# Performance work log

Measured on AMD Instinct MI355X. Metric: run time of the kernel, lower is better.

## Reference

```python
import jax, jax.numpy as jnp
import numpy as np


def _xavier(key, shape):
    fan_out, fan_in = shape
    lim = float(np.sqrt(6.0 / (fan_in + fan_out)))
    return jax.random.uniform(key, shape, jnp.float32, -lim, lim)


def setup_inputs() -> dict:
    B, I, H, P = 8192, 1024, 1024, 2048
    key = jax.random.key(0)
    ks = jax.random.split(key, 12)
    return {
        "x": jax.random.normal(ks[0], (B, I), jnp.float32),
        "hidden": jax.random.normal(ks[1], (B, H), jnp.float32),
        "persistent_memory": jax.random.normal(ks[2], (B, P), jnp.float32),
        # attention_gate: Linear(H,H), 'gate' bias init = -0.1
        "Wa": _xavier(ks[3], (H, H)), "ba": jnp.full((H,), -0.1, jnp.float32),
        # reset/update/new gates: Linear(I+H, H), 'gate' bias init = -0.1
        "Wr": _xavier(ks[4], (H, I + H)), "br": jnp.full((H,), -0.1, jnp.float32),
        "Wu": _xavier(ks[5], (H, I + H)), "bu": jnp.full((H,), -0.1, jnp.float32),
        "Wn": _xavier(ks[6], (H, I + H)), "bn": jnp.full((H,), -0.1, jnp.float32),
        # memory read/write/address: Linear(H,P), zero bias; forget bias = 1.0
        "Wread": _xavier(ks[7], (P, H)), "bread": jnp.zeros((P,), jnp.float32),
        "Wwrite": _xavier(ks[8], (P, H)), "bwrite": jnp.zeros((P,), jnp.float32),
        "Wforget": _xavier(ks[9], (P, H)), "bforget": jnp.ones((P,), jnp.float32),
        "Waddr": _xavier(ks[10], (P, H)), "baddr": jnp.zeros((P,), jnp.float32),
        "connection_strength": jnp.ones((H,), jnp.float32),
        "connection_decay": jnp.full((1,), 0.99, jnp.float32),
        "connection_history": jnp.zeros((H,), jnp.float32),  # buffer, starts at 0
    }


def reference(x, hidden, persistent_memory, Wa, ba, Wr, br, Wu, bu, Wn, bn,
              Wread, bread, Wwrite, bwrite, Wforget, bforget, Waddr, baddr,
              connection_strength, connection_decay, connection_history):
    H = hidden.shape[1]
    # update_connections (reward=None): history*decay + detached mean(|h|) over batch
    activity = jax.lax.stop_gradient(jnp.mean(jnp.abs(hidden), axis=0))  # [H]
    ch = connection_history * connection_decay + activity
    cs = connection_strength * jax.nn.sigmoid(ch)  # [H]

    attention = jax.nn.sigmoid(hidden @ Wa.T + ba)
    ha = hidden * attention
    combined = jnp.concatenate([x, ha], axis=1)
    reset = combined @ Wr.T + br
    update = combined @ Wu.T + bu
    combined_reset = jnp.concatenate([x, reset * ha], axis=1)
    new = combined_reset @ Wn.T + bn
    # neuromodulators=None: apply_neuromodulation returns gates UNACTIVATED (faithful)
    hidden_new = (1.0 - update) * hidden + update * new * cs[None, :]  # [B,H]

    addr = jax.nn.softmax(hidden_new @ Waddr.T + baddr, axis=1)        # [B,P]
    read = jax.nn.sigmoid(hidden_new @ Wread.T + bread)
    write = jax.nn.sigmoid(hidden_new @ Wwrite.T + bwrite)
    forget = jax.nn.sigmoid(hidden_new @ Wforget.T + bforget)

    # F.linear with ones(P,H)/H weight == row-mean of hidden_new broadcast to P
    hp = jnp.mean(hidden_new, axis=1, keepdims=True)                   # [B,1]
    memory_new = forget * persistent_memory + write * hp * addr        # [B,P]
    memory_read_content = read * memory_new
    # F.linear with ones(H,P)/P weight == row-mean over P broadcast to H
    hidden_final = hidden_new + jnp.mean(memory_read_content, axis=1, keepdims=True)
    return hidden_final, memory_new
```

## Files before the change

kernel.cpp:

```cpp
#include <hip/hip_runtime.h>

typedef unsigned short u16;
typedef short bfrag __attribute__((ext_vector_type(8)));
typedef float f32x4 __attribute__((ext_vector_type(4)));
typedef const __attribute__((address_space(1))) unsigned int* gp1_t;
typedef __attribute__((address_space(3))) unsigned int* lp3_t;

#define B_ 8192
#define H_ 1024
#define P_ 2048

__device__ __forceinline__ u16 f2bf(float f) {
  unsigned u = __builtin_bit_cast(unsigned, f);
  u += 0x7fffu + ((u >> 16) & 1u);
  return (u16)(u >> 16);
}
__device__ __forceinline__ float bf2f(u16 s) {
  return __builtin_bit_cast(float, (unsigned)s << 16);
}
__device__ __forceinline__ float sigm(float v) { return 1.f / (1.f + __expf(-v)); }


__global__ void k_hidact(const float* __restrict__ hidden, u16* __restrict__ hB,
                         float* __restrict__ act) {
  const int t = threadIdx.x;
  const int r0 = blockIdx.x * 16;
  float s00 = 0, s01 = 0, s10 = 0, s11 = 0;
  for (int r = 0; r < 16; ++r) {
    const float* q = hidden + (size_t)(r0 + r) * H_;
    u16* o = hB + (size_t)(r0 + r) * H_;
    float2 v0 = *(const float2*)&q[2 * t];
    float2 v1 = *(const float2*)&q[512 + 2 * t];
    s00 += fabsf(v0.x); s01 += fabsf(v0.y);
    s10 += fabsf(v1.x); s11 += fabsf(v1.y);
    ushort2 o0, o1;
    o0.x = f2bf(v0.x); o0.y = f2bf(v0.y);
    o1.x = f2bf(v1.x); o1.y = f2bf(v1.y);
    *(ushort2*)&o[2 * t] = o0;
    *(ushort2*)&o[512 + 2 * t] = o1;
  }
  atomicAdd(&act[2 * t], s00); atomicAdd(&act[2 * t + 1], s01);
  atomicAdd(&act[512 + 2 * t], s10); atomicAdd(&act[512 + 2 * t + 1], s11);
}

__global__ void k_cs(const float* __restrict__ act, const float* __restrict__ strength,
                     const float* __restrict__ decay, const float* __restrict__ hist,
                     float* __restrict__ cs) {
  int h = blockIdx.x * 256 + threadIdx.x;
  float ch = hist[h] * decay[0] + act[h] * (1.f / (float)B_);
  cs[h] = strength[h] * sigm(ch);
}

struct ConvPs {
  const float* s[9];
  u16* d[9];
  int n4[9];
};

__global__ void k_conv9(ConvPs p) {
  const int e = blockIdx.y;
  const int n4 = p.n4[e];
  const float4* s = (const float4*)p.s[e];
  ushort4* d = (ushort4*)p.d[e];
  for (int i = blockIdx.x * 256 + threadIdx.x; i < n4; i += 2048 * 256) {
    float4 v = s[i];
    ushort4 o;
    o.x = f2bf(v.x); o.y = f2bf(v.y); o.z = f2bf(v.z); o.w = f2bf(v.w);
    d[i] = o;
  }
}

__global__ void k_rowmean(const float* __restrict__ hn, float* __restrict__ hp) {
  int row = blockIdx.x * 4 + (threadIdx.x >> 6);
  int lane = threadIdx.x & 63;
  const float4* p4 = (const float4*)(hn + (size_t)row * H_);
  float s = 0.f;
#pragma unroll
  for (int c = 0; c < 4; ++c) {
    float4 v = p4[lane + c * 64];
    s += v.x + v.y + v.z + v.w;
  }
#pragma unroll
  for (int o = 32; o; o >>= 1) s += __shfl_down(s, o);
  if (lane == 0) hp[row] = s * (1.f / (float)H_);
}


struct GemmPs {
  const u16* Bm[4];
  const float* bias[4];
  const float* hidden;
  const float* update;
  const float* cs;
  const u16* haB;
  u16* rhaB;
  float* out_f1;
  float* hn_f32;
  u16* hn_bf16;
  u16* haB_out;
  u16* out_b[4];
};

template <int EPI>
__device__ __forceinline__ void epiV(int row, int col0, f32x4 v, int z, const GemmPs& e) {
  if constexpr (EPI == 1) {
    float4 bi = *(const float4*)&e.bias[0][col0];
    size_t i = (size_t)row * H_ + col0;
    float4 hd = *(const float4*)&e.hidden[i];
    ushort4 o;
    o.x = f2bf(hd.x * sigm(v[0] + bi.x));
    o.y = f2bf(hd.y * sigm(v[1] + bi.y));
    o.z = f2bf(hd.z * sigm(v[2] + bi.z));
    o.w = f2bf(hd.w * sigm(v[3] + bi.w));
    *(ushort4*)&e.haB_out[i] = o;
  } else if constexpr (EPI == 2) {
    size_t i = (size_t)row * H_ + col0;
    if (z == 0) {
      float4 bi = *(const float4*)&e.bias[0][col0];
      ushort4 h = *(const ushort4*)&e.haB[i];
      ushort4 o;
      o.x = f2bf((v[0] + bi.x) * bf2f(h.x));
      o.y = f2bf((v[1] + bi.y) * bf2f(h.y));
      o.z = f2bf((v[2] + bi.z) * bf2f(h.z));
      o.w = f2bf((v[3] + bi.w) * bf2f(h.w));
      *(ushort4*)&e.rhaB[i] = o;
    } else {
      float4 bi = *(const float4*)&e.bias[1][col0];
      float4 o;
      o.x = v[0] + bi.x; o.y = v[1] + bi.y; o.z = v[2] + bi.z; o.w = v[3] + bi.w;
      *(float4*)&e.out_f1[i] = o;
    }
  } else if constexpr (EPI == 3) {
    float4 bi = *(const float4*)&e.bias[0][col0];
    size_t i = (size_t)row * H_ + col0;
    float4 u4 = *(const float4*)&e.update[i];
    float4 hd = *(const float4*)&e.hidden[i];
    float4 c4 = *(const float4*)&e.cs[col0];
    float4 hn;
    hn.x = (1.f - u4.x) * hd.x + u4.x * (v[0] + bi.x) * c4.x;
    hn.y = (1.f - u4.y) * hd.y + u4.y * (v[1] + bi.y) * c4.y;
    hn.z = (1.f - u4.z) * hd.z + u4.z * (v[2] + bi.z) * c4.z;
    hn.w = (1.f - u4.w) * hd.w + u4.w * (v[3] + bi.w) * c4.w;
    *(float4*)&e.hn_f32[i] = hn;
    ushort4 o;
    o.x = f2bf(hn.x); o.y = f2bf(hn.y); o.z = f2bf(hn.z); o.w = f2bf(hn.w);
    *(ushort4*)&e.hn_bf16[i] = o;
  } else {
    float4 bi = *(const float4*)&e.bias[z][col0];
    ushort4 o;
    o.x = f2bf(v[0] + bi.x); o.y = f2bf(v[1] + bi.y);
    o.z = f2bf(v[2] + bi.z); o.w = f2bf(v[3] + bi.w);
    *(ushort4*)&e.out_b[z][(size_t)row * P_ + col0] = o;
  }
}


template <int EPI, int KB, int NT0, int NT1>
__global__ __launch_bounds__(256, 2) void gemm_bt(const u16* __restrict__ A0,
                                                  const u16* __restrict__ A1,
                                                  GemmPs e) {
  const int z = blockIdx.z;
  const u16* __restrict__ Bm = e.Bm[z];
  __shared__ u16 As[128 * 64];
  __shared__ u16 Bs[128 * 64];
  const int lane = threadIdx.x & 63;
  const int w = threadIdx.x >> 6;
  const int wr = w >> 1, wc = w & 1;
  const int m0 = blockIdx.x * 128, n0 = blockIdx.y * 128;

  f32x4 acc[4][4] = {};

  const int rA = lane >> 3;
  const int srcSlot8 = ((lane & 7) ^ (rA & 7)) << 3;
  const int g = lane >> 4;
  const int r15 = lane & 15;
  const int rx = lane & 7;

  const u16* pA0 = A0 + (size_t)(m0 + w * 32 + rA) * H_ + srcSlot8;
  const u16* pA1 = A1 + (size_t)(m0 + w * 32 + rA) * H_ + srcSlot8;
  const u16* pB  = Bm + (size_t)(n0 + w * 32 + rA) * KB + srcSlot8;

  auto ktile = [&](const u16* pAk, const u16* pBk) {
#pragma unroll
    for (int j = 0; j < 4; ++j) {
      __builtin_amdgcn_global_load_lds((gp1_t)(pAk + (size_t)(j * 8) * H_),
                                       (lp3_t)&As[(w * 32 + j * 8) * 64], 16, 0, 0);
      __builtin_amdgcn_global_load_lds((gp1_t)(pBk + (size_t)(j * 8) * KB),
                                       (lp3_t)&Bs[(w * 32 + j * 8) * 64], 16, 0, 0);
    }
    asm volatile("s_waitcnt vmcnt(0)" ::: "memory");
    __syncthreads();
#pragma unroll
    for (int kk = 0; kk < 2; ++kk) {
      const int cswz = (((g + kk * 4) ^ rx) << 3);
      bfrag af[4], bq[4];
#pragma unroll
      for (int i = 0; i < 4; ++i) {
        af[i] = *(const bfrag*)&As[(wr * 64 + i * 16 + r15) * 64 + cswz];
        bq[i] = *(const bfrag*)&Bs[(wc * 64 + i * 16 + r15) * 64 + cswz];
      }
#pragma unroll
      for (int mi = 0; mi < 4; ++mi)
#pragma unroll
        for (int ni = 0; ni < 4; ++ni)
          acc[mi][ni] = __builtin_amdgcn_mfma_f32_16x16x32_bf16(bq[ni], af[mi], acc[mi][ni], 0, 0, 0);
    }
    __syncthreads();
  };

  for (int t = 0; t < NT0; ++t) ktile(pA0 + t * 64, pB + t * 64);
  if constexpr (NT1 > 0)
    for (int t = 0; t < NT1; ++t) ktile(pA1 + t * 64, pB + (NT0 + t) * 64);

#pragma unroll
  for (int mi = 0; mi < 4; ++mi)
#pragma unroll
    for (int ni = 0; ni < 4; ++ni)
      epiV<EPI>(m0 + wr * 64 + mi * 16 + r15,
                n0 + wc * 64 + ni * 16 + g * 4, acc[mi][ni], z, e);
}


__global__ __launch_bounds__(256) void k_final(
    const u16* __restrict__ aL, const u16* __restrict__ rL,
    const u16* __restrict__ wL, const u16* __restrict__ fL,
    const float* __restrict__ pm, const float* __restrict__ hn,
    const float* __restrict__ hp, float* __restrict__ outH, float* __restrict__ outM) {
  __shared__ float red[8];
  const int row = blockIdx.x, t = threadIdx.x;
  const size_t base = (size_t)row * P_ + t * 8;

  ushort4 a0 = *(const ushort4*)&aL[base];
  ushort4 a1 = *(const ushort4*)&aL[base + 4];
  float av[8] = {bf2f(a0.x), bf2f(a0.y), bf2f(a0.z), bf2f(a0.w),
                 bf2f(a1.x), bf2f(a1.y), bf2f(a1.z), bf2f(a1.w)};
  float lm = av[0];
#pragma unroll
  for (int j = 1; j < 8; ++j) lm = fmaxf(lm, av[j]);
#pragma unroll
  for (int o = 32; o; o >>= 1) lm = fmaxf(lm, __shfl_xor(lm, o));
  if ((t & 63) == 0) red[t >> 6] = lm;
  __syncthreads();
  const float bmax = fmaxf(fmaxf(red[0], red[1]), fmaxf(red[2], red[3]));

  float ev[8];
  float ls = 0.f;
#pragma unroll
  for (int j = 0; j < 8; ++j) { ev[j] = __expf(av[j] - bmax); ls += ev[j]; }
#pragma unroll
  for (int o = 32; o; o >>= 1) ls += __shfl_xor(ls, o);
  if ((t & 63) == 0) red[4 + (t >> 6)] = ls;
  __syncthreads();
  const float inv = 1.f / (red[4] + red[5] + red[6] + red[7]);
  const float hpv = hp[row];

  ushort4 r0 = *(const ushort4*)&rL[base], r1 = *(const ushort4*)&rL[base + 4];
  ushort4 w0 = *(const ushort4*)&wL[base], w1 = *(const ushort4*)&wL[base + 4];
  ushort4 f0 = *(const ushort4*)&fL[base], f1 = *(const ushort4*)&fL[base + 4];
  float4 p0 = *(const float4*)&pm[base], p1 = *(const float4*)&pm[base + 4];
  float rv[8] = {bf2f(r0.x), bf2f(r0.y), bf2f(r0.z), bf2f(r0.w),
                 bf2f(r1.x), bf2f(r1.y), bf2f(r1.z), bf2f(r1.w)};
  float wv[8] = {bf2f(w0.x), bf2f(w0.y), bf2f(w0.z), bf2f(w0.w),
                 bf2f(w1.x), bf2f(w1.y), bf2f(w1.z), bf2f(w1.w)};
  float fv[8] = {bf2f(f0.x), bf2f(f0.y), bf2f(f0.z), bf2f(f0.w),
                 bf2f(f1.x), bf2f(f1.y), bf2f(f1.z), bf2f(f1.w)};
  float pv[8] = {p0.x, p0.y, p0.z, p0.w, p1.x, p1.y, p1.z, p1.w};
  float mem[8];
  float rs = 0.f;
#pragma unroll
  for (int j = 0; j < 8; ++j) {
    mem[j] = sigm(fv[j]) * pv[j] + sigm(wv[j]) * hpv * (ev[j] * inv);
    rs += sigm(rv[j]) * mem[j];
  }
  float4 m0v = {mem[0], mem[1], mem[2], mem[3]};
  float4 m1v = {mem[4], mem[5], mem[6], mem[7]};
  *(float4*)&outM[base] = m0v;
  *(float4*)&outM[base + 4] = m1v;
#pragma unroll
  for (int o = 32; o; o >>= 1) rs += __shfl_xor(rs, o);
  __syncthreads();
  if ((t & 63) == 0) red[t >> 6] = rs;
  __syncthreads();
  const float mean = (red[0] + red[1] + red[2] + red[3]) * (1.f / (float)P_);
  const size_t hb = (size_t)row * H_ + t * 4;
  float4 h4 = *(const float4*)&hn[hb];
  h4.x += mean; h4.y += mean; h4.z += mean; h4.w += mean;
  *(float4*)&outH[hb] = h4;
}


extern "C" void kernel_launch(void* const* d_in, const int* in_sizes, int n_in,
                              void* d_out, int out_size, void* d_ws, size_t ws_size,
                              hipStream_t stream) {
  (void)in_sizes; (void)n_in; (void)out_size; (void)ws_size;
  const float* x       = (const float*)d_in[0];
  const float* hidden  = (const float*)d_in[1];
  const float* pm      = (const float*)d_in[2];
  const float* Wa      = (const float*)d_in[3];
  const float* ba      = (const float*)d_in[4];
  const float* Wr      = (const float*)d_in[5];
  const float* br      = (const float*)d_in[6];
  const float* Wu      = (const float*)d_in[7];
  const float* bu      = (const float*)d_in[8];
  const float* Wn      = (const float*)d_in[9];
  const float* bn      = (const float*)d_in[10];
  const float* Wread   = (const float*)d_in[11];
  const float* bread   = (const float*)d_in[12];
  const float* Wwrite  = (const float*)d_in[13];
  const float* bwrite  = (const float*)d_in[14];
  const float* Wforget = (const float*)d_in[15];
  const float* bforget = (const float*)d_in[16];
  const float* Waddr   = (const float*)d_in[17];
  const float* baddr   = (const float*)d_in[18];
  const float* cstr    = (const float*)d_in[19];
  const float* cdecay  = (const float*)d_in[20];
  const float* chist   = (const float*)d_in[21];

  char* wsp = (char*)d_ws;
  auto take = [&](size_t n) { char* p = wsp; wsp += (n + 255) & ~(size_t)255; return p; };
  float* act    = (float*)take((size_t)H_ * 4);
  float* cs     = (float*)take((size_t)H_ * 4);
  float* hp     = (float*)take((size_t)B_ * 4);
  u16* hiddenB  = (u16*)take((size_t)B_ * H_ * 2);
  u16* xB       = (u16*)take((size_t)B_ * H_ * 2);
  u16* haB      = (u16*)take((size_t)B_ * H_ * 2);
  u16* rhaB     = (u16*)take((size_t)B_ * H_ * 2);
  u16* WaB      = (u16*)take((size_t)H_ * H_ * 2);
  u16* WrB      = (u16*)take((size_t)H_ * 2048 * 2);
  u16* WuB      = (u16*)take((size_t)H_ * 2048 * 2);
  u16* WnB      = (u16*)take((size_t)H_ * 2048 * 2);
  u16* WadB     = (u16*)take((size_t)P_ * H_ * 2);
  u16* WrdB     = (u16*)take((size_t)P_ * H_ * 2);
  u16* WwrB     = (u16*)take((size_t)P_ * H_ * 2);
  u16* WfgB     = (u16*)take((size_t)P_ * H_ * 2);
  float* update = (float*)take((size_t)B_ * H_ * 4);
  float* hnf    = (float*)take((size_t)B_ * H_ * 4);
  u16* gAd      = (u16*)take((size_t)B_ * P_ * 2);
  u16* gRd      = (u16*)take((size_t)B_ * P_ * 2);
  u16* gWr      = (u16*)take((size_t)B_ * P_ * 2);
  u16* gFg      = (u16*)take((size_t)B_ * P_ * 2);

  float* outH = (float*)d_out;
  float* outM = outH + (size_t)B_ * H_;

  hipMemsetAsync(act, 0, (size_t)H_ * 4, stream);
  k_hidact<<<dim3(512), dim3(256), 0, stream>>>(hidden, hiddenB, act);
  k_cs<<<dim3(4), dim3(256), 0, stream>>>(act, cstr, cdecay, chist, cs);

  {
    ConvPs p;
    const float* ss[9] = {Wa, Wr, Wu, Wn, Waddr, Wread, Wwrite, Wforget, x};
    u16* dd[9] = {WaB, WrB, WuB, WnB, WadB, WrdB, WwrB, WfgB, xB};
    int nn[9] = {H_ * H_ / 4, H_ * 2048 / 4, H_ * 2048 / 4, H_ * 2048 / 4,
                 P_ * H_ / 4, P_ * H_ / 4, P_ * H_ / 4, P_ * H_ / 4, B_ * H_ / 4};
    for (int i = 0; i < 9; ++i) { p.s[i] = ss[i]; p.d[i] = dd[i]; p.n4[i] = nn[i]; }
    k_conv9<<<dim3(2048, 9), dim3(256), 0, stream>>>(p);
  }

  {
    GemmPs e{};
    e.Bm[0] = WaB; e.bias[0] = ba; e.hidden = hidden; e.haB_out = haB;
    gemm_bt<1, 1024, 16, 0><<<dim3(64, 8, 1), dim3(256), 0, stream>>>(hiddenB, hiddenB, e);
  }
  {
    GemmPs e{};
    e.Bm[0] = WrB; e.Bm[1] = WuB; e.bias[0] = br; e.bias[1] = bu;
    e.haB = haB; e.rhaB = rhaB; e.out_f1 = update;
    gemm_bt<2, 2048, 16, 16><<<dim3(64, 8, 2), dim3(256), 0, stream>>>(xB, haB, e);
  }
  {
    GemmPs e{};
    e.Bm[0] = WnB; e.bias[0] = bn; e.hidden = hidden; e.update = update; e.cs = cs;
    e.hn_f32 = hnf; e.hn_bf16 = hiddenB;
    gemm_bt<3, 2048, 16, 16><<<dim3(64, 8, 1), dim3(256), 0, stream>>>(xB, rhaB, e);
  }
  k_rowmean<<<dim3(2048), dim3(256), 0, stream>>>(hnf, hp);
  {
    GemmPs e{};
    e.Bm[0] = WadB; e.Bm[1] = WrdB; e.Bm[2] = WwrB; e.Bm[3] = WfgB;
    e.bias[0] = baddr; e.bias[1] = bread; e.bias[2] = bwrite; e.bias[3] = bforget;
    e.out_b[0] = gAd; e.out_b[1] = gRd; e.out_b[2] = gWr; e.out_b[3] = gFg;
    gemm_bt<4, 1024, 16, 0><<<dim3(64, 16, 4), dim3(256), 0, stream>>>(hiddenB, hiddenB, e);
  }
  k_final<<<dim3(B_), dim3(256), 0, stream>>>(gAd, gRd, gWr, gFg, pm, hnf, hp, outH, outM);
}
```

Before: 432.1 us.

## Fuse hidden_new row-mean into GEMM epilogue and drop fp32 hidden_new buffer

The hidden_new row-sum is now accumulated in the Wn GEMM epilogue through wave shuffles and atomics into hp, which removes the separate rowmean kernel. The fp32 hidden_new buffer is dropped, so the final kernel reads the bf16 copy instead. That saves a 32MB write and read but costs precision in hidden_final. The hidden activity/convert kernel is also reshaped to use float4 accesses with 64 rows per block.

Measured after the change: 403.5 us. 1.07x faster.

```diff
diff --git a/kernel.cpp b/kernel.cpp
--- a/kernel.cpp
+++ b/kernel.cpp
@@ -24,23 +24,18 @@
 __global__ void k_hidact(const float* __restrict__ hidden, u16* __restrict__ hB,
                          float* __restrict__ act) {
   const int t = threadIdx.x;
-  const int r0 = blockIdx.x * 16;
-  float s00 = 0, s01 = 0, s10 = 0, s11 = 0;
-  for (int r = 0; r < 16; ++r) {
-    const float* q = hidden + (size_t)(r0 + r) * H_;
-    u16* o = hB + (size_t)(r0 + r) * H_;
-    float2 v0 = *(const float2*)&q[2 * t];
-    float2 v1 = *(const float2*)&q[512 + 2 * t];
-    s00 += fabsf(v0.x); s01 += fabsf(v0.y);
-    s10 += fabsf(v1.x); s11 += fabsf(v1.y);
-    ushort2 o0, o1;
-    o0.x = f2bf(v0.x); o0.y = f2bf(v0.y);
-    o1.x = f2bf(v1.x); o1.y = f2bf(v1.y);
-    *(ushort2*)&o[2 * t] = o0;
-    *(ushort2*)&o[512 + 2 * t] = o1;
-  }
-  atomicAdd(&act[2 * t], s00); atomicAdd(&act[2 * t + 1], s01);
-  atomicAdd(&act[512 + 2 * t], s10); atomicAdd(&act[512 + 2 * t + 1], s11);
+  const int r0 = blockIdx.x * 64;
+  float s0 = 0, s1 = 0, s2 = 0, s3 = 0;
+  for (int r = 0; r < 64; ++r) {
+    const size_t i = (size_t)(r0 + r) * H_ + t * 4;
+    float4 v = *(const float4*)&hidden[i];
+    s0 += fabsf(v.x); s1 += fabsf(v.y); s2 += fabsf(v.z); s3 += fabsf(v.w);
+    ushort4 o;
+    o.x = f2bf(v.x); o.y = f2bf(v.y); o.z = f2bf(v.z); o.w = f2bf(v.w);
+    *(ushort4*)&hB[i] = o;
+  }
+  atomicAdd(&act[t * 4], s0); atomicAdd(&act[t * 4 + 1], s1);
+  atomicAdd(&act[t * 4 + 2], s2); atomicAdd(&act[t * 4 + 3], s3);
 }
 
 __global__ void k_cs(const float* __restrict__ act, const float* __restrict__ strength,
@@ -68,21 +63,6 @@
     o.x = f2bf(v.x); o.y = f2bf(v.y); o.z = f2bf(v.z); o.w = f2bf(v.w);
     d[i] = o;
   }
-}
-
-__global__ void k_rowmean(const float* __restrict__ hn, float* __restrict__ hp) {
-  int row = blockIdx.x * 4 + (threadIdx.x >> 6);
-  int lane = threadIdx.x & 63;
-  const float4* p4 = (const float4*)(hn + (size_t)row * H_);
-  float s = 0.f;
-#pragma unroll
-  for (int c = 0; c < 4; ++c) {
-    float4 v = p4[lane + c * 64];
-    s += v.x + v.y + v.z + v.w;
-  }
-#pragma unroll
-  for (int o = 32; o; o >>= 1) s += __shfl_down(s, o);
-  if (lane == 0) hp[row] = s * (1.f / (float)H_);
 }
 
 
@@ -95,14 +75,14 @@
   const u16* haB;
   u16* rhaB;
   float* out_f1;
-  float* hn_f32;
   u16* hn_bf16;
+  float* hp;
   u16* haB_out;
   u16* out_b[4];
 };
 
 template <int EPI>
-__device__ __forceinline__ void epiV(int row, int col0, f32x4 v, int z, const GemmPs& e) {
+__device__ __forceinline__ float epiV(int row, int col0, f32x4 v, int z, const GemmPs& e) {
   if constexpr (EPI == 1) {
     float4 bi = *(const float4*)&e.bias[0][col0];
     size_t i = (size_t)row * H_ + col0;
@@ -113,6 +93,7 @@
     o.z = f2bf(hd.z * sigm(v[2] + bi.z));
     o.w = f2bf(hd.w * sigm(v[3] + bi.w));
     *(ushort4*)&e.haB_out[i] = o;
+    return 0.f;
   } else if constexpr (EPI == 2) {
     size_t i = (size_t)row * H_ + col0;
     if (z == 0) {
@@ -130,27 +111,28 @@
       o.x = v[0] + bi.x; o.y = v[1] + bi.y; o.z = v[2] + bi.z; o.w = v[3] + bi.w;
       *(float4*)&e.out_f1[i] = o;
     }
+    return 0.f;
   } else if constexpr (EPI == 3) {
     float4 bi = *(const float4*)&e.bias[0][col0];
     size_t i = (size_t)row * H_ + col0;
     float4 u4 = *(const float4*)&e.update[i];
     float4 hd = *(const float4*)&e.hidden[i];
     float4 c4 = *(const float4*)&e.cs[col0];
-    float4 hn;
-    hn.x = (1.f - u4.x) * hd.x + u4.x * (v[0] + bi.x) * c4.x;
-    hn.y = (1.f - u4.y) * hd.y + u4.y * (v[1] + bi.y) * c4.y;
-    hn.z = (1.f - u4.z) * hd.z + u4.z * (v[2] + bi.z) * c4.z;
-    hn.w = (1.f - u4.w) * hd.w + u4.w * (v[3] + bi.w) * c4.w;
-    *(float4*)&e.hn_f32[i] = hn;
-    ushort4 o;
-    o.x = f2bf(hn.x); o.y = f2bf(hn.y); o.z = f2bf(hn.z); o.w = f2bf(hn.w);
+    float hx = (1.f - u4.x) * hd.x + u4.x * (v[0] + bi.x) * c4.x;
+    float hy = (1.f - u4.y) * hd.y + u4.y * (v[1] + bi.y) * c4.y;
+    float hz = (1.f - u4.z) * hd.z + u4.z * (v[2] + bi.z) * c4.z;
+    float hw = (1.f - u4.w) * hd.w + u4.w * (v[3] + bi.w) * c4.w;
+    ushort4 o;
+    o.x = f2bf(hx); o.y = f2bf(hy); o.z = f2bf(hz); o.w = f2bf(hw);
     *(ushort4*)&e.hn_bf16[i] = o;
+    return hx + hy + hz + hw;
   } else {
     float4 bi = *(const float4*)&e.bias[z][col0];
     ushort4 o;
     o.x = f2bf(v[0] + bi.x); o.y = f2bf(v[1] + bi.y);
     o.z = f2bf(v[2] + bi.z); o.w = f2bf(v[3] + bi.w);
     *(ushort4*)&e.out_b[z][(size_t)row * P_ + col0] = o;
+    return 0.f;
   }
 }
 
@@ -212,19 +194,38 @@
   if constexpr (NT1 > 0)
     for (int t = 0; t < NT1; ++t) ktile(pA1 + t * 64, pB + (NT0 + t) * 64);
 
-#pragma unroll
-  for (int mi = 0; mi < 4; ++mi)
-#pragma unroll
-    for (int ni = 0; ni < 4; ++ni)
-      epiV<EPI>(m0 + wr * 64 + mi * 16 + r15,
-                n0 + wc * 64 + ni * 16 + g * 4, acc[mi][ni], z, e);
+  if constexpr (EPI == 3) {
+    float rsum[4];
+#pragma unroll
+    for (int mi = 0; mi < 4; ++mi) {
+      rsum[mi] = 0.f;
+#pragma unroll
+      for (int ni = 0; ni < 4; ++ni)
+        rsum[mi] += epiV<EPI>(m0 + wr * 64 + mi * 16 + r15,
+                              n0 + wc * 64 + ni * 16 + g * 4, acc[mi][ni], z, e);
+    }
+#pragma unroll
+    for (int mi = 0; mi < 4; ++mi) {
+      float s = rsum[mi];
+      s += __shfl_xor(s, 16);
+      s += __shfl_xor(s, 32);
+      if (g == 0) atomicAdd(&e.hp[m0 + wr * 64 + mi * 16 + r15], s);
+    }
+  } else {
+#pragma unroll
+    for (int mi = 0; mi < 4; ++mi)
+#pragma unroll
+      for (int ni = 0; ni < 4; ++ni)
+        epiV<EPI>(m0 + wr * 64 + mi * 16 + r15,
+                  n0 + wc * 64 + ni * 16 + g * 4, acc[mi][ni], z, e);
+  }
 }
 
 
 __global__ __launch_bounds__(256) void k_final(
     const u16* __restrict__ aL, const u16* __restrict__ rL,
     const u16* __restrict__ wL, const u16* __restrict__ fL,
-    const float* __restrict__ pm, const float* __restrict__ hn,
+    const float* __restrict__ pm, const u16* __restrict__ hnB,
     const float* __restrict__ hp, float* __restrict__ outH, float* __restrict__ outM) {
   __shared__ float red[8];
   const int row = blockIdx.x, t = threadIdx.x;
@@ -252,7 +253,7 @@
   if ((t & 63) == 0) red[4 + (t >> 6)] = ls;
   __syncthreads();
   const float inv = 1.f / (red[4] + red[5] + red[6] + red[7]);
-  const float hpv = hp[row];
+  const float hpv = hp[row] * (1.f / (float)H_);
 
   ushort4 r0 = *(const ushort4*)&rL[base], r1 = *(const ushort4*)&rL[base + 4];
   ushort4 w0 = *(const ushort4*)&wL[base], w1 = *(const ushort4*)&wL[base + 4];
@@ -283,9 +284,11 @@
   __syncthreads();
   const float mean = (red[0] + red[1] + red[2] + red[3]) * (1.f / (float)P_);
   const size_t hb = (size_t)row * H_ + t * 4;
-  float4 h4 = *(const float4*)&hn[hb];
-  h4.x += mean; h4.y += mean; h4.z += mean; h4.w += mean;
-  *(float4*)&outH[hb] = h4;
+  ushort4 h4 = *(const ushort4*)&hnB[hb];
+  float4 o4;
+  o4.x = bf2f(h4.x) + mean; o4.y = bf2f(h4.y) + mean;
+  o4.z = bf2f(h4.z) + mean; o4.w = bf2f(h4.w) + mean;
+  *(float4*)&outH[hb] = o4;
 }
 
 
@@ -319,8 +322,8 @@
   char* wsp = (char*)d_ws;
   auto take = [&](size_t n) { char* p = wsp; wsp += (n + 255) & ~(size_t)255; return p; };
   float* act    = (float*)take((size_t)H_ * 4);
+  float* hp     = (float*)take((size_t)B_ * 4);
   float* cs     = (float*)take((size_t)H_ * 4);
-  float* hp     = (float*)take((size_t)B_ * 4);
   u16* hiddenB  = (u16*)take((size_t)B_ * H_ * 2);
   u16* xB       = (u16*)take((size_t)B_ * H_ * 2);
   u16* haB      = (u16*)take((size_t)B_ * H_ * 2);
@@ -334,7 +337,6 @@
   u16* WwrB     = (u16*)take((size_t)P_ * H_ * 2);
   u16* WfgB     = (u16*)take((size_t)P_ * H_ * 2);
   float* update = (float*)take((size_t)B_ * H_ * 4);
-  float* hnf    = (float*)take((size_t)B_ * H_ * 4);
   u16* gAd      = (u16*)take((size_t)B_ * P_ * 2);
   u16* gRd      = (u16*)take((size_t)B_ * P_ * 2);
   u16* gWr      = (u16*)take((size_t)B_ * P_ * 2);
@@ -343,8 +345,8 @@
   float* outH = (float*)d_out;
   float* outM = outH + (size_t)B_ * H_;
 
-  hipMemsetAsync(act, 0, (size_t)H_ * 4, stream);
-  k_hidact<<<dim3(512), dim3(256), 0, stream>>>(hidden, hiddenB, act);
+  hipMemsetAsync(act, 0, (size_t)H_ * 4 + (size_t)B_ * 4, stream);
+  k_hidact<<<dim3(128), dim3(256), 0, stream>>>(hidden, hiddenB, act);
   k_cs<<<dim3(4), dim3(256), 0, stream>>>(act, cstr, cdecay, chist, cs);
 
   {
@@ -371,10 +373,9 @@
   {
     GemmPs e{};
     e.Bm[0] = WnB; e.bias[0] = bn; e.hidden = hidden; e.update = update; e.cs = cs;
-    e.hn_f32 = hnf; e.hn_bf16 = hiddenB;
+    e.hn_bf16 = hiddenB; e.hp = hp;
     gemm_bt<3, 2048, 16, 16><<<dim3(64, 8, 1), dim3(256), 0, stream>>>(xB, rhaB, e);
   }
-  k_rowmean<<<dim3(2048), dim3(256), 0, stream>>>(hnf, hp);
   {
     GemmPs e{};
     e.Bm[0] = WadB; e.Bm[1] = WrdB; e.Bm[2] = WwrB; e.Bm[3] = WfgB;
@@ -382,5 +383,5 @@
     e.out_b[0] = gAd; e.out_b[1] = gRd; e.out_b[2] = gWr; e.out_b[3] = gFg;
     gemm_bt<4, 1024, 16, 0><<<dim3(64, 16, 4), dim3(256), 0, stream>>>(hiddenB, hiddenB, e);
   }
-  k_final<<<dim3(B_), dim3(256), 0, stream>>>(gAd, gRd, gWr, gFg, pm, hnf, hp, outH, outM);
-}
+  k_final<<<dim3(B_), dim3(256), 0, stream>>>(gAd, gRd, gWr, gFg, pm, hiddenB, hp, outH, outM);
+}
```
